# Kernel tuning notes

Hardware: AMD Instinct MI355X
Metric: run time of the kernel (lower is better)

## Reference

```python
import jax, jax.numpy as jnp
import numpy as np

B = 64
NS = [5024, 1257, 315, 80, 21]  # padded vertex counts per mesh level
K = 9                            # spiral length
LAT = 256


def _sconv(x, idx, W, b, elu=True):
    # x: [B, N, F], idx: [N, K] spiral neighbor indices -> gather, GEMM, activation, zero-pad mask
    Bq, N, _ = x.shape
    g = x[:, idx.reshape(-1), :].reshape(Bq, N, -1)  # [B, N, K*F]
    o = g @ W + b
    if elu:
        o = jax.nn.elu(o)
    return o.at[:, -1, :].set(0.0)  # zero the padding vertex


def _pool(M, x):
    # M: [M_out, M_in] dense down/up-sample matrix
    return jnp.einsum('mn,bnf->bmf', M, x)


def _forward(x, s0, s1, s2, s3, D0, D1, D2, D3, U0, U1, U2, U3,
             We0, be0, We1, be1, We2, be2, We3, be3,
             fceW, fceb, fcdW, fcdb,
             Wd0, bd0, Wd1, bd1, Wd2, bd2, Wd3, bd3):
    # encoder: spiral conv + downsample at each level
    h = _pool(D0, _sconv(x, s0, We0, be0))
    h = _pool(D1, _sconv(h, s1, We1, be1))
    h = _pool(D2, _sconv(h, s2, We2, be2))
    h = _pool(D3, _sconv(h, s3, We3, be3))
    z = h.reshape(h.shape[0], -1) @ fceW + fceb          # [B, LAT]
    # decoder: upsample + spiral conv, last conv has identity activation
    h = (z @ fcdW + fcdb).reshape(z.shape[0], NS[4], -1)  # [B, 21, 256]
    h = _sconv(_pool(U3, h), s3, Wd0, bd0)
    h = _sconv(_pool(U2, h), s2, Wd1, bd1)
    h = _sconv(_pool(U1, h), s1, Wd2, bd2)
    h = _sconv(_pool(U0, h), s0, Wd3, bd3, elu=False)
    return h  # [B, 5024, 3]


def setup_inputs() -> dict:
    key = jax.random.key(0)
    ks = iter(jax.random.split(key, 64))
    nrm = lambda shape, s=0.05: jax.random.normal(next(ks), shape, dtype=jnp.float32) * s
    d = {}
    d['x'] = jax.random.normal(next(ks), (B, NS[0], 3), dtype=jnp.float32)
    for i in range(4):
        n = NS[i]
        d[f's{i}'] = jax.random.randint(next(ks), (n, K), 0, n, dtype=jnp.int32).astype(jnp.int64)
    for i in range(4):
        d[f'D{i}'] = nrm((NS[i + 1], NS[i]))
        d[f'U{i}'] = nrm((NS[i], NS[i + 1]))
    enc = [(3, 64), (64, 64), (64, 128), (128, 256)]
    for i, (fi, fo) in enumerate(enc):
        d[f'We{i}'] = nrm((fi * K, fo))
        d[f'be{i}'] = jnp.zeros((fo,), jnp.float32)
    d['fceW'] = nrm((NS[4] * 256, LAT))
    d['fceb'] = jnp.zeros((LAT,), jnp.float32)
    d['fcdW'] = nrm((LAT, NS[4] * 256))
    d['fcdb'] = jnp.zeros((NS[4] * 256,), jnp.float32)
    dec = [(256, 128), (128, 64), (64, 64), (64, 3)]
    for i, (fi, fo) in enumerate(dec):
        d[f'Wd{i}'] = nrm((fi * K, fo))
        d[f'bd{i}'] = jnp.zeros((fo,), jnp.float32)
    return d


def reference(x, s0, s1, s2, s3, D0, D1, D2, D3, U0, U1, U2, U3,
              We0, be0, We1, be1, We2, be2, We3, be3,
              fceW, fceb, fcdW, fcdb,
              Wd0, bd0, Wd1, bd1, Wd2, bd2, Wd3, bd3):
    return _forward(x, s0, s1, s2, s3, D0, D1, D2, D3, U0, U1, U2, U3,
                    We0, be0, We1, be1, We2, be2, We3, be3,
                    fceW, fceb, fcdW, fcdb,
                    Wd0, bd0, Wd1, bd1, Wd2, bd2, Wd3, bd3)
```

## Files before the change

kernel.cpp:

```cpp
#include <hip/hip_runtime.h>
#include <math.h>

typedef __attribute__((ext_vector_type(8))) _Float16 half8;
typedef __attribute__((ext_vector_type(4))) _Float16 half4;
typedef __attribute__((ext_vector_type(4))) float f32x4;
typedef unsigned long long u64;

#define BK 32

#define EPI_NAT  0
#define EPI_TR   1
#define EPI_FCD  2
#define EPI_OUT  3
#define EPI_PART 4

typedef const __attribute__((address_space(1))) void* gas1;
typedef __attribute__((address_space(3))) void* las3;

__device__ __forceinline__ void gl16(const void* g, void* l) {
    __builtin_amdgcn_global_load_lds((gas1)g, (las3)l, 16, 0, 0);
}
template<int N> __device__ __forceinline__ void vwait() {
    asm volatile("s_waitcnt vmcnt(%0)" :: "n"(N) : "memory");
}
__device__ __forceinline__ void barx() {
    asm volatile("" ::: "memory");
    __builtin_amdgcn_s_barrier();
    asm volatile("" ::: "memory");
}

__global__ __launch_bounds__(256, 3) void pool4_k(
    const _Float16* __restrict__ Aw, const _Float16* __restrict__ Bw,
    _Float16* __restrict__ Cp, int M, int Np, u64 c_rs)
{
    constexpr int LPS = 6;

    __shared__ _Float16 sA[2][64][64];
    __shared__ _Float16 sB[2][128][64];

    const int t  = threadIdx.x;
    const int m0 = blockIdx.y * 64;
    const int f0 = blockIdx.x * 128;
    const int lane = t & 63;
    const int wid  = t >> 6;
    const int wm = wid >> 1;
    const int wf = wid & 1;
    const int lm = lane & 15;
    const int lg = lane >> 4;

    f32x4 acc[2][4];
    #pragma unroll
    for (int i = 0; i < 2; ++i)
        #pragma unroll
        for (int j = 0; j < 4; ++j)
            acc[i][j] = (f32x4)0.0f;

    auto stage = [&](int buf, int ks) {
        #pragma unroll
        for (int j = 0; j < 2; ++j) {
            int c   = t + j * 256;
            int row = c >> 3;
            int ch  = (c & 7) ^ (row & 7);
            int rc  = m0 + row; if (rc >= M) rc = M - 1;
            gl16(Aw + (u64)rc * Np + ks * 64 + ch * 8,
                 (_Float16*)&sA[buf][0][0] + (u64)c * 8);
        }
        #pragma unroll
        for (int j = 0; j < 4; ++j) {
            int c   = t + j * 256;
            int row = c >> 3;
            int ch  = (c & 7) ^ (row & 7);
            gl16(Bw + (u64)(f0 + row) * Np + ks * 64 + ch * 8,
                 (_Float16*)&sB[buf][0][0] + (u64)c * 8);
        }
    };

    auto compute = [&](int buf) {
        #pragma unroll
        for (int kh = 0; kh < 2; ++kh) {
            const int ch = (kh * 4 + lg) ^ (lm & 7);
            half8 af[2], bf[4];
            #pragma unroll
            for (int i = 0; i < 2; ++i)
                af[i] = *(const half8*)&sA[buf][wm * 32 + i * 16 + lm][ch * 8];
            #pragma unroll
            for (int j = 0; j < 4; ++j)
                bf[j] = *(const half8*)&sB[buf][wf * 64 + j * 16 + lm][ch * 8];
            #pragma unroll
            for (int i = 0; i < 2; ++i)
                #pragma unroll
                for (int j = 0; j < 4; ++j)
                    acc[i][j] = __builtin_amdgcn_mfma_f32_16x16x32_f16(af[i], bf[j], acc[i][j], 0, 0, 0);
        }
    };

    const int ke = Np / 64;
    stage(0, 0);
    if (1 < ke) stage(1, 1);
    for (int ks = 0; ks < ke; ++ks) {
        if (ke - ks >= 2) vwait<LPS>();
        else              vwait<0>();
        barx();
        compute(ks & 1);
        barx();
        if (ks + 2 < ke) stage(ks & 1, ks + 2);
    }

    #pragma unroll
    for (int j = 0; j < 4; ++j) {
        int fl = f0 + wf * 64 + j * 16 + lm;
        #pragma unroll
        for (int i = 0; i < 2; ++i) {
            #pragma unroll
            for (int r = 0; r < 4; ++r) {
                int m = m0 + wm * 32 + i * 16 + lg * 4 + r;
                if (m < M)
                    Cp[(u64)m * c_rs + fl] = (_Float16)acc[i][j][r];
            }
        }
    }
}

template<int TBM>
__global__ __launch_bounds__(256, 3) void pool2_k(
    const _Float16* __restrict__ Aw, const _Float16* __restrict__ Bw,
    _Float16* __restrict__ Cp, int M, int Np, u64 c_rs)
{
    constexpr int FM  = TBM / 32;
    constexpr int LPS = TBM / 64 + 2;

    __shared__ _Float16 sA[3][TBM][BK];
    __shared__ _Float16 sB[3][128][BK];

    const int t  = threadIdx.x;
    const int m0 = blockIdx.y * TBM;
    const int f0 = blockIdx.x * 128;
    const int lane = t & 63;
    const int wid  = t >> 6;
    const int wm = wid >> 1;
    const int wf = wid & 1;
    const int lm = lane & 15;
    const int lg = lane >> 4;

    f32x4 acc[FM][4];
    #pragma unroll
    for (int i = 0; i < FM; ++i)
        #pragma unroll
        for (int j = 0; j < 4; ++j)
            acc[i][j] = (f32x4)0.0f;

    auto stage = [&](int buf, int ks) {
        #pragma unroll
        for (int j = 0; j < TBM / 64; ++j) {
            int c   = t + j * 256;
            int row = c >> 2;
            int sw  = ((c & 3) ^ ((row >> 1) & 3)) * 8;
            int rc  = m0 + row; if (rc >= M) rc = M - 1;
            gl16(Aw + (u64)rc * Np + ks * BK + sw,
                 (_Float16*)&sA[buf][0][0] + (u64)c * 8);
        }
        #pragma unroll
        for (int j = 0; j < 2; ++j) {
            int c   = t + j * 256;
            int row = c >> 2;
            int sw  = ((c & 3) ^ ((row >> 1) & 3)) * 8;
            gl16(Bw + (u64)(f0 + row) * Np + ks * BK + sw,
                 (_Float16*)&sB[buf][0][0] + (u64)c * 8);
        }
    };

    auto compute = [&](int buf) {
        const int sa = (lg ^ ((lm >> 1) & 3)) * 8;
        half8 af[FM], bf[4];
        #pragma unroll
        for (int i = 0; i < FM; ++i)
            af[i] = *(const half8*)&sA[buf][wm * (FM * 16) + i * 16 + lm][sa];
        #pragma unroll
        for (int j = 0; j < 4; ++j)
            bf[j] = *(const half8*)&sB[buf][wf * 64 + j * 16 + lm][sa];
        #pragma unroll
        for (int i = 0; i < FM; ++i)
            #pragma unroll
            for (int j = 0; j < 4; ++j)
                acc[i][j] = __builtin_amdgcn_mfma_f32_16x16x32_f16(af[i], bf[j], acc[i][j], 0, 0, 0);
    };

    const int ke = Np / BK;
    stage(0, 0);
    if (1 < ke) stage(1, 1);
    if (2 < ke) stage(2, 2);
    int cur = 0;
    for (int ks = 0; ks < ke; ++ks) {
        int rem = ke - ks;
        if (rem >= 3)      vwait<2 * LPS>();
        else if (rem == 2) vwait<LPS>();
        else               vwait<0>();
        barx();
        compute(cur);
        barx();
        if (ks + 3 < ke) stage(cur, ks + 3);
        cur = (cur == 2) ? 0 : cur + 1;
    }

    #pragma unroll
    for (int j = 0; j < 4; ++j) {
        int fl = f0 + wf * 64 + j * 16 + lm;
        #pragma unroll
        for (int i = 0; i < FM; ++i) {
            #pragma unroll
            for (int r = 0; r < 4; ++r) {
                int m = m0 + wm * (FM * 16) + i * 16 + lg * 4 + r;
                if (m < M)
                    Cp[(u64)m * c_rs + fl] = (_Float16)acc[i][j][r];
            }
        }
    }
}

template<int AMODE, int EPI, int TBM, int TBF, int WM, int WF>
__global__ __launch_bounds__(256) void gemm_k(
    const _Float16* __restrict__ Aw, u64 a_rs,
    const int* __restrict__ idx, int FiLog,
    const _Float16* __restrict__ Bw,
    const float* __restrict__ bias,
    void* __restrict__ Cp, u64 c_rs, int Mp_out,
    int M, int Np, int F, int flags, int ksp)
{
    constexpr int FM = TBM / WM / 16;
    constexpr int FF = TBF / WF / 16;
    constexpr int LPS_A = TBM / 64;
    constexpr bool BSM = (TBF < 64);
    constexpr int LPS_B = BSM ? 0 : TBF / 64;
    constexpr int LW0 = LPS_A + (BSM ? 1 : LPS_B);
    constexpr int LWX = LPS_A + LPS_B;
    constexpr int NI = (AMODE == 1 || AMODE == 2) ? TBM : 2;

    __shared__ _Float16 sA[3][TBM][BK];
    __shared__ _Float16 sB[3][TBF][BK];
    __shared__ int sIdx[NI][9];

    const int t  = threadIdx.x;
    const int b  = blockIdx.z;
    const int m0 = blockIdx.y * TBM;
    const int f0 = blockIdx.x * TBF;
    const int lane = t & 63;
    const int wid  = t >> 6;
    const int wm = wid / WF;
    const int wf = wid % WF;
    const int lm = lane & 15;
    const int lg = lane >> 4;
    const int Fi = 1 << FiLog;

    f32x4 acc[FM][FF];
    #pragma unroll
    for (int i = 0; i < FM; ++i)
        #pragma unroll
        for (int j = 0; j < FF; ++j)
            acc[i][j] = (f32x4)0.0f;

    if constexpr (AMODE == 1 || AMODE == 2) {
        for (int i = t; i < TBM * 9; i += 256) {
            int r = i / 9, k = i - r * 9;
            int rc = m0 + r; if (rc >= M) rc = M - 1;
            sIdx[r][k] = idx[rc * 9 + k];
        }
        __syncthreads();
    } else if constexpr (AMODE == 5) {
        if (t < 18) {
            int r = t / 9, k = t - r * 9;
            sIdx[r][k] = idx[((m0 >> 6) + r) * 9 + k];
        }
        __syncthreads();
    }

    auto stage = [&](int buf, int ks) {
        if constexpr (AMODE != 2) {
            #pragma unroll
            for (int j = 0; j < LPS_A; ++j) {
                int c   = t + j * 256;
                int row = c >> 2;
                int sw  = ((c & 3) ^ ((row >> 1) & 3)) * 8;
                int col = ks * BK + sw;
                const _Float16* src;
                if constexpr (AMODE == 3) {
                    int rc = m0 + row; if (rc >= M) rc = M - 1;
                    src = Aw + (u64)rc * Np + col;
                } else if constexpr (AMODE == 1) {
                    int k = col >> FiLog, fi = col & (Fi - 1);
                    src = Aw + (u64)sIdx[row][k] * a_rs + b * Fi + fi;
                } else if constexpr (AMODE == 4) {
                    int k = col >> FiLog, fi = col & (Fi - 1);
                    src = Aw + (u64)k * a_rs + (m0 + row) * Fi + fi;
                } else {
                    int k = col >> FiLog, fi = col & (Fi - 1);
                    int bb = (m0 + row) & 63;
                    src = Aw + (u64)sIdx[row >> 6][k] * a_rs + bb * Fi + fi;
                }
                gl16(src, &sA[buf][row][(c & 3) * 8]);
            }
        }
        if constexpr (!BSM) {
            #pragma unroll
            for (int j = 0; j < LPS_B; ++j) {
                int c   = t + j * 256;
                int row = c >> 2;
                int sw  = ((c & 3) ^ ((row >> 1) & 3)) * 8;
                gl16(Bw + (u64)(f0 + row) * Np + ks * BK + sw, &sB[buf][row][(c & 3) * 8]);
            }
        } else {
            if (wid == 0) {
                int c   = t;
                int row = c >> 2;
                int sw  = ((c & 3) ^ ((row >> 1) & 3)) * 8;
                gl16(Bw + (u64)(f0 + row) * Np + ks * BK + sw, &sB[buf][row][(c & 3) * 8]);
            }
        }
    };

    auto compute = [&](int buf) {
        const int sa = (lg ^ ((lm >> 1) & 3)) * 8;
        half8 af[FM], bf[FF];
        #pragma unroll
        for (int i = 0; i < FM; ++i)
            af[i] = *(const half8*)&sA[buf][wm * (FM * 16) + i * 16 + lm][sa];
        #pragma unroll
        for (int j = 0; j < FF; ++j)
            bf[j] = *(const half8*)&sB[buf][wf * (FF * 16) + j * 16 + lm][sa];
        #pragma unroll
        for (int i = 0; i < FM; ++i)
            #pragma unroll
            for (int j = 0; j < FF; ++j)
                acc[i][j] = __builtin_amdgcn_mfma_f32_16x16x32_f16(af[i], bf[j], acc[i][j], 0, 0, 0);
    };

    if constexpr (AMODE == 2) {
        stage(0, 0);
        stage(1, 1);
        {
            int row = t >> 1;
            int h   = t & 1;
            #pragma unroll
            for (int cc = 0; cc < 4; ++cc) {
                int g0 = h * 8 + cc * 2;
                int g1 = g0 + 1;
                half4 lo = {(_Float16)0,(_Float16)0,(_Float16)0,(_Float16)0};
                half4 hi = lo;
                if (g0 < 9) lo = *(const half4*)(Aw + (u64)sIdx[row][g0] * a_rs + b * 4);
                if (g1 < 9) hi = *(const half4*)(Aw + (u64)sIdx[row][g1] * a_rs + b * 4);
                half8 w;
                #pragma unroll
                for (int q = 0; q < 4; ++q) { w[q] = lo[q]; w[4 + q] = hi[q]; }
                int cp = cc ^ ((row >> 1) & 3);
                *(half8*)&sA[h][row][cp * 8] = w;
            }
        }
        vwait<0>();
        __syncthreads();
        compute(0);
        compute(1);
    } else {
        int kb = 0, ke = Np / BK;
        if constexpr (AMODE == 4) { kb = b * ksp; ke = kb + ksp; }
        stage(0, kb);
        if (kb + 1 < ke) stage(1, kb + 1);
        if (kb + 2 < ke) stage(2, kb + 2);
        int cur = 0;
        for (int ks = kb; ks < ke; ++ks) {
            int rem = ke - ks;
            if (rem >= 3) {
                if constexpr (LW0 == LWX) vwait<2 * LW0>();
                else { if (wid == 0) vwait<2 * LW0>(); else vwait<2 * LWX>(); }
            } else if (rem == 2) {
                if constexpr (LW0 == LWX) vwait<LW0>();
                else { if (wid == 0) vwait<LW0>(); else vwait<LWX>(); }
            } else {
                vwait<0>();
            }
            barx();
            compute(cur);
            barx();
            if (ks + 3 < ke) stage(cur, ks + 3);
            cur = (cur == 2) ? 0 : cur + 1;
        }
    }

    if constexpr (EPI == EPI_TR) {
        #pragma unroll
        for (int j = 0; j < FF; ++j) {
            int fl = f0 + wf * (FF * 16) + j * 16 + lm;
            float bv = (bias != nullptr && fl < F) ? bias[fl] : 0.f;
            #pragma unroll
            for (int i = 0; i < FM; ++i) {
                int mb = m0 + wm * (FM * 16) + i * 16 + lg * 4;
                if (fl < F && mb < Mp_out) {
                    half4 o;
                    #pragma unroll
                    for (int r = 0; r < 4; ++r) {
                        int m = mb + r;
                        float v = acc[i][j][r] + bv;
                        if (flags & 1) v = (v > 0.f) ? v : expm1f(v);
                        o[r] = (m < M && !((flags & 2) && m == M - 1)) ? (_Float16)v : (_Float16)0.f;
                    }
                    *(half4*)&((_Float16*)Cp)[(u64)b * c_rs + (u64)fl * Mp_out + mb] = o;
                }
            }
        }
    } else {
        #pragma unroll
        for (int j = 0; j < FF; ++j) {
            int fl = f0 + wf * (FF * 16) + j * 16 + lm;
            float bv = 0.f;
            if (bias != nullptr && fl < F) bv = bias[fl];
            #pragma unroll
            for (int i = 0; i < FM; ++i) {
                #pragma unroll
                for (int r = 0; r < 4; ++r) {
                    int m = m0 + wm * (FM * 16) + i * 16 + lg * 4 + r;
                    float v = acc[i][j][r] + bv;
                    if (flags & 1) v = (v > 0.f) ? v : expm1f(v);
                    if constexpr (EPI == EPI_NAT) {
                        if (m < M && fl < F)
                            ((_Float16*)Cp)[(u64)m * c_rs + fl] = (_Float16)v;
                    } else if constexpr (EPI == EPI_FCD) {
                        if (m < M && fl < F)
                            ((_Float16*)Cp)[((u64)m * 256 + (fl & 255)) * 32 + (fl >> 8)] = (_Float16)v;
                    } else if constexpr (EPI == EPI_PART) {
                        if (m < M && fl < F)
                            ((float*)Cp)[(u64)b * c_rs + (u64)m * F + fl] = v;
                    } else {
                        if (m < M && fl < F) {
                            int vo = m >> 6, bb = m & 63;
                            float o = ((flags & 2) && vo == Mp_out - 1) ? 0.f : v;
                            ((float*)Cp)[((u64)bb * Mp_out + vo) * 3 + fl] = o;
                        }
                    }
                }
            }
        }
    }
}

struct CvtPtrs { const float* p[18]; };

constexpr int CV_R[18]  = {1257,5024,315,1257,80,315,21,80,  64,64,128,256,256,5376,128,64,64,16};
constexpr int CV_N[18]  = {5024,1257,1257,315,315,80,80,21,  27,576,576,1152,5376,256,2304,1152,576,576};
constexpr int CV_NP[18] = {5120,1280,1280,320,320,96,96,32,  64,576,576,1152,5376,256,2304,1152,576,576};
constexpr int CV_F[18]  = {0,0,0,0,0,0,0,0,  64,64,128,256,256,5376,128,64,64,3};

constexpr u64 cv_elems(int i) { return (u64)CV_R[i] * CV_NP[i]; }
constexpr u64 cv_off(int i) { u64 o = 0; for (int j = 0; j < i; ++j) o += (cv_elems(j) + 255) & ~(u64)255; return o; }
constexpr int cv_blk(int i) { return (int)((cv_elems(i) + 255) >> 8); }
constexpr int cv_start(int i) { int s = 0; for (int j = 0; j < i; ++j) s += cv_blk(j); return s; }

__global__ __launch_bounds__(256) void cvt_all(CvtPtrs ps, _Float16* __restrict__ dst)
{
    const int bx = blockIdx.x, t = threadIdx.x;
    #pragma unroll
    for (int i = 0; i < 18; ++i) {
        if (bx >= cv_start(i) && bx < cv_start(i + 1)) {
            const u64 e = (u64)(bx - cv_start(i)) * 256 + t;
            if (e < cv_elems(i)) {
                const int NP = CV_NP[i], N = CV_N[i], Fo = CV_F[i];
                int row = (int)(e / (u64)NP);
                int col = (int)(e - (u64)row * NP);
                float v = 0.f;
                const float* s = ps.p[i];
                if (i == 8) {
                    int k = col >> 2, c = col & 3;
                    if (c < 3 && k < 9) v = s[(u64)(k * 3 + c) * Fo + row];
                } else if (Fo == 0) {
                    if (col < N) v = s[(u64)row * N + col];
                } else {
                    if (col < N && row < Fo) v = s[(u64)col * Fo + row];
                }
                dst[cv_off(i) + e] = (_Float16)v;
            }
        }
    }
}

__global__ void cvt_x(const float* __restrict__ src, _Float16* __restrict__ dst)
{
    int i = blockIdx.x * 256 + threadIdx.x;
    if (i >= 5024 * 256) return;
    int v = i >> 8;
    int r = i & 255;
    int b = r >> 2, c = r & 3;
    dst[i] = (c < 3) ? (_Float16)src[((u64)b * 5024 + v) * 3 + c] : (_Float16)0.f;
}

__global__ void reduce_fce(const float* __restrict__ part, const float* __restrict__ bias,
                           _Float16* __restrict__ z)
{
    int i = blockIdx.x * 256 + threadIdx.x;
    int fl = i & 255;
    float s = bias[fl];
    #pragma unroll
    for (int p = 0; p < 8; ++p) s += part[(u64)p * 16384 + i];
    z[i] = (_Float16)s;
}

extern "C" void kernel_launch(void* const* d_in, const int* in_sizes, int n_in,
                              void* d_out, int out_size, void* d_ws, size_t ws_size,
                              hipStream_t stream)
{
    const float* x  = (const float*)d_in[0];
    const int* s0 = (const int*)d_in[1];
    const int* s1 = (const int*)d_in[2];
    const int* s2 = (const int*)d_in[3];
    const int* s3 = (const int*)d_in[4];
    const float* be0 = (const float*)d_in[14];
    const float* be1 = (const float*)d_in[16];
    const float* be2 = (const float*)d_in[18];
    const float* be3 = (const float*)d_in[20];
    const float* fceb = (const float*)d_in[22];
    const float* fcdb = (const float*)d_in[24];
    const float* bd0 = (const float*)d_in[26];
    const float* bd1 = (const float*)d_in[28];
    const float* bd2 = (const float*)d_in[30];
    const float* bd3 = (const float*)d_in[32];

    _Float16* W = (_Float16*)d_ws;
    size_t off = 0;
    auto alloc = [&](size_t e) { size_t o = off; off += (e + 255) & ~(size_t)255; return o; };

    const size_t oActV = alloc((size_t)5024 * 4096);
    const size_t oActT = alloc((size_t)4096 * 5120);
    const size_t oZ    = alloc((size_t)64 * 256);
    const size_t oPart = alloc((size_t)8 * 64 * 256 * 2);
    const size_t oU3in = alloc((size_t)16384 * 32);
    const size_t oXp   = alloc((size_t)5024 * 256);
    const size_t oCvt  = alloc((size_t)(cv_off(17) + ((cv_elems(17) + 255) & ~(u64)255)));
    auto wofs = [&](int i) { return oCvt + (size_t)cv_off(i); };

    cvt_x<<<dim3(5024), 256, 0, stream>>>(x, W + oXp);
    {
        CvtPtrs ps;
        ps.p[0] = (const float*)d_in[5];
        ps.p[1] = (const float*)d_in[6];
        ps.p[2] = (const float*)d_in[7];
        ps.p[3] = (const float*)d_in[8];
        ps.p[4] = (const float*)d_in[9];
        ps.p[5] = (const float*)d_in[10];
        ps.p[6] = (const float*)d_in[11];
        ps.p[7] = (const float*)d_in[12];
        ps.p[8] = (const float*)d_in[13];
        ps.p[9] = (const float*)d_in[15];
        ps.p[10] = (const float*)d_in[17];
        ps.p[11] = (const float*)d_in[19];
        ps.p[12] = (const float*)d_in[21];
        ps.p[13] = (const float*)d_in[23];
        ps.p[14] = (const float*)d_in[25];
        ps.p[15] = (const float*)d_in[27];
        ps.p[16] = (const float*)d_in[29];
        ps.p[17] = (const float*)d_in[31];
        cvt_all<<<dim3(cv_start(18)), 256, 0, stream>>>(ps, W + oCvt);
    }
    hipMemsetAsync(W + oU3in, 0, (size_t)16384 * 32 * sizeof(_Float16), stream);

    #define GEMM(AM, EP, BM_, BF_, WM_, WF_, gx, gy, gz, Aw_, ars_, idx_, FiL_, Bw_, bias_, Cp_, crs_, Mp_, M_, Np_, F_, fl_, ksp_) \
        gemm_k<AM, EP, BM_, BF_, WM_, WF_><<<dim3(gx, gy, gz), 256, 0, stream>>>( \
            Aw_, ars_, idx_, FiL_, Bw_, bias_, Cp_, crs_, Mp_, M_, Np_, F_, fl_, ksp_)
    #define POOL(TBM_, gx, gy, Aw_, Bw_, Cp_, M_, Np_, crs_) \
        pool2_k<TBM_><<<dim3(gx, gy), 256, 0, stream>>>(Aw_, Bw_, Cp_, M_, Np_, crs_)
    #define POOL4(gx, gy, Aw_, Bw_, Cp_, M_, Np_, crs_) \
        pool4_k<<<dim3(gx, gy), 256, 0, stream>>>(Aw_, Bw_, Cp_, M_, Np_, crs_)

    GEMM(2, EPI_TR, 128, 64, 2, 2, 1, 40, 64, W + oXp, 256, s0, 0,
         W + wofs(8), be0, W + oActT, (u64)64 * 5120, 5120, 5024, 64, 64, 3, 0);
    POOL4(32, 20, W + wofs(0), W + oActT, W + oActV, 1257, 5120, 4096);
    GEMM(1, EPI_TR, 128, 64, 2, 2, 1, 10, 64, W + oActV, 4096, s1, 6,
         W + wofs(9), be1, W + oActT, (u64)64 * 1280, 1280, 1257, 576, 64, 3, 0);
    POOL(64, 32, 5, W + wofs(2), W + oActT, W + oActV, 315, 1280, 4096);
    GEMM(1, EPI_TR, 128, 64, 2, 2, 2, 3, 64, W + oActV, 4096, s2, 6,
         W + wofs(10), be2, W + oActT, (u64)128 * 320, 320, 315, 576, 128, 3, 0);
    POOL(64, 64, 2, W + wofs(4), W + oActT, W + oActV, 80, 320, 8192);
    GEMM(1, EPI_TR, 128, 64, 2, 2, 4, 1, 64, W + oActV, 8192, s3, 7,
         W + wofs(11), be3, W + oActT, (u64)256 * 96, 96, 80, 1152, 256, 3, 0);
    POOL(64, 128, 1, W + wofs(6), W + oActT, W + oActV, 21, 96, 16384);
    GEMM(4, EPI_PART, 64, 64, 2, 2, 4, 1, 8, W + oActV, 16384, nullptr, 8,
         W + wofs(12), nullptr, W + oPart, (u64)64 * 256, 0, 64, 5376, 256, 0, 21);
    reduce_fce<<<dim3(64), 256, 0, stream>>>((const float*)(W + oPart), fceb, W + oZ);
    GEMM(3, EPI_FCD, 64, 128, 2, 2, 42, 1, 1, W + oZ, 0, nullptr, 0,
         W + wofs(13), fcdb, W + oU3in, 0, 0, 64, 256, 5376, 0, 0);
    POOL(64, 128, 2, W + wofs(7), W + oU3in, W + oActV, 80, 32, 16384);
    GEMM(1, EPI_TR, 128, 64, 2, 2, 2, 1, 64, W + oActV, 16384, s3, 8,
         W + wofs(14), bd0, W + oActT, (u64)128 * 96, 96, 80, 2304, 128, 3, 0);
    POOL(64, 64, 5, W + wofs(5), W + oActT, W + oActV, 315, 96, 8192);
    GEMM(1, EPI_TR, 128, 64, 2, 2, 1, 3, 64, W + oActV, 8192, s2, 7,
         W + wofs(15), bd1, W + oActT, (u64)64 * 320, 320, 315, 1152, 64, 3, 0);
    POOL4(32, 20, W + wofs(3), W + oActT, W + oActV, 1257, 320, 4096);
    GEMM(1, EPI_TR, 128, 64, 2, 2, 1, 10, 64, W + oActV, 4096, s1, 6,
         W + wofs(16), bd2, W + oActT, (u64)64 * 1280, 1280, 1257, 576, 64, 3, 0);
    POOL4(32, 79, W + wofs(1), W + oActT, W + oActV, 5024, 1280, 4096);
    GEMM(5, EPI_OUT, 128, 16, 4, 1, 1, 2512, 1, W + oActV, 4096, s0, 6,
         W + wofs(17), bd3, d_out, 0, 5024, 321536, 576, 3, 2, 0);
    #undef GEMM
    #undef POOL
    #undef POOL4
}
```

Measured before the change: 505.8 us.

## Add dedicated spiral-conv GEMM kernel with BK=64 double buffering and wider MFMA

Adds a specialised sconv4_k kernel for the gathered spiral-convolution GEMMs. It uses a 64-wide K tile with double buffering, an XOR-swizzled LDS layout and the 16x16x32 f16 MFMA, and writes vectorised half4 outputs with a fused bias/ELU/pad-zero epilogue. It replaces the generic gemm_k AMODE 1 path for six conv layers and moves two pooling launches to the pool4 kernel. The aim is fewer K iterations and barriers plus cheaper stores. In exchange it requires Np to be a multiple of 64 and holds more LDS per block.

```diff
diff --git a/kernel.cpp b/kernel.cpp
--- a/kernel.cpp
+++ b/kernel.cpp
@@ -116,6 +116,123 @@
                 int m = m0 + wm * 32 + i * 16 + lg * 4 + r;
                 if (m < M)
                     Cp[(u64)m * c_rs + fl] = (_Float16)acc[i][j][r];
+            }
+        }
+    }
+}
+
+template<int TBM, int TBF, int WM, int WF>
+__global__ __launch_bounds__(256) void sconv4_k(
+    const _Float16* __restrict__ Aw, u64 a_rs,
+    const int* __restrict__ idx, int FiLog,
+    const _Float16* __restrict__ Bw,
+    const float* __restrict__ bias,
+    _Float16* __restrict__ Cp, u64 c_rs, int Mp_out,
+    int M, int Np, int F, int flags)
+{
+    constexpr int FM = TBM / WM / 16;
+    constexpr int FF = TBF / WF / 16;
+    constexpr int LPS = TBM / 32 + TBF / 32;
+
+    __shared__ _Float16 sA[2][TBM][64];
+    __shared__ _Float16 sB[2][TBF][64];
+    __shared__ int sIdx[TBM][9];
+
+    const int t  = threadIdx.x;
+    const int b  = blockIdx.z;
+    const int m0 = blockIdx.y * TBM;
+    const int f0 = blockIdx.x * TBF;
+    const int lane = t & 63;
+    const int wid  = t >> 6;
+    const int wm = wid / WF;
+    const int wf = wid % WF;
+    const int lm = lane & 15;
+    const int lg = lane >> 4;
+    const int Fi = 1 << FiLog;
+
+    f32x4 acc[FM][FF];
+    #pragma unroll
+    for (int i = 0; i < FM; ++i)
+        #pragma unroll
+        for (int j = 0; j < FF; ++j)
+            acc[i][j] = (f32x4)0.0f;
+
+    for (int i = t; i < TBM * 9; i += 256) {
+        int r = i / 9, k = i - r * 9;
+        int rc = m0 + r; if (rc >= M) rc = M - 1;
+        sIdx[r][k] = idx[rc * 9 + k];
+    }
+    __syncthreads();
+
+    auto stage = [&](int buf, int ks) {
+        #pragma unroll
+        for (int j = 0; j < TBM / 32; ++j) {
+            int c   = t + j * 256;
+            int row = c >> 3;
+            int ch  = (c & 7) ^ (row & 7);
+            int col = ks * 64 + ch * 8;
+            int k = col >> FiLog, fi = col & (Fi - 1);
+            gl16(Aw + (u64)sIdx[row][k] * a_rs + b * Fi + fi,
+                 (_Float16*)&sA[buf][0][0] + (u64)c * 8);
+        }
+        #pragma unroll
+        for (int j = 0; j < TBF / 32; ++j) {
+            int c   = t + j * 256;
+            int row = c >> 3;
+            int ch  = (c & 7) ^ (row & 7);
+            gl16(Bw + (u64)(f0 + row) * Np + ks * 64 + ch * 8,
+                 (_Float16*)&sB[buf][0][0] + (u64)c * 8);
+        }
+    };
+
+    auto compute = [&](int buf) {
+        #pragma unroll
+        for (int kh = 0; kh < 2; ++kh) {
+            const int ch = (kh * 4 + lg) ^ (lm & 7);
+            half8 af[FM], bf[FF];
+            #pragma unroll
+            for (int i = 0; i < FM; ++i)
+                af[i] = *(const half8*)&sA[buf][wm * (FM * 16) + i * 16 + lm][ch * 8];
+            #pragma unroll
+            for (int j = 0; j < FF; ++j)
+                bf[j] = *(const half8*)&sB[buf][wf * (FF * 16) + j * 16 + lm][ch * 8];
+            #pragma unroll
+            for (int i = 0; i < FM; ++i)
+                #pragma unroll
+                for (int j = 0; j < FF; ++j)
+                    acc[i][j] = __builtin_amdgcn_mfma_f32_16x16x32_f16(af[i], bf[j], acc[i][j], 0, 0, 0);
+        }
+    };
+
+    const int ke = Np / 64;
+    stage(0, 0);
+    if (1 < ke) stage(1, 1);
+    for (int ks = 0; ks < ke; ++ks) {
+        if (ke - ks >= 2) vwait<LPS>();
+        else              vwait<0>();
+        barx();
+        compute(ks & 1);
+        barx();
+        if (ks + 2 < ke) stage(ks & 1, ks + 2);
+    }
+
+    #pragma unroll
+    for (int j = 0; j < FF; ++j) {
+        int fl = f0 + wf * (FF * 16) + j * 16 + lm;
+        float bv = (bias != nullptr && fl < F) ? bias[fl] : 0.f;
+        #pragma unroll
+        for (int i = 0; i < FM; ++i) {
+            int mb = m0 + wm * (FM * 16) + i * 16 + lg * 4;
+            if (fl < F && mb < Mp_out) {
+                half4 o;
+                #pragma unroll
+                for (int r = 0; r < 4; ++r) {
+                    int m = mb + r;
+                    float v = acc[i][j][r] + bv;
+                    if (flags & 1) v = (v > 0.f) ? v : expm1f(v);
+                    o[r] = (m < M && !((flags & 2) && m == M - 1)) ? (_Float16)v : (_Float16)0.f;
+                }
+                *(half4*)&Cp[(u64)b * c_rs + (u64)fl * Mp_out + mb] = o;
             }
         }
     }
@@ -233,7 +350,7 @@
     constexpr int LPS_B = BSM ? 0 : TBF / 64;
     constexpr int LW0 = LPS_A + (BSM ? 1 : LPS_B);
     constexpr int LWX = LPS_A + LPS_B;
-    constexpr int NI = (AMODE == 1 || AMODE == 2) ? TBM : 2;
+    constexpr int NI = (AMODE == 2) ? TBM : 2;
 
     __shared__ _Float16 sA[3][TBM][BK];
     __shared__ _Float16 sB[3][TBF][BK];
@@ -258,7 +375,7 @@
         for (int j = 0; j < FF; ++j)
             acc[i][j] = (f32x4)0.0f;
 
-    if constexpr (AMODE == 1 || AMODE == 2) {
+    if constexpr (AMODE == 2) {
         for (int i = t; i < TBM * 9; i += 256) {
             int r = i / 9, k = i - r * 9;
             int rc = m0 + r; if (rc >= M) rc = M - 1;
@@ -285,9 +402,6 @@
                 if constexpr (AMODE == 3) {
                     int rc = m0 + row; if (rc >= M) rc = M - 1;
                     src = Aw + (u64)rc * Np + col;
-                } else if constexpr (AMODE == 1) {
-                    int k = col >> FiLog, fi = col & (Fi - 1);
-                    src = Aw + (u64)sIdx[row][k] * a_rs + b * Fi + fi;
                 } else if constexpr (AMODE == 4) {
                     int k = col >> FiLog, fi = col & (Fi - 1);
                     src = Aw + (u64)k * a_rs + (m0 + row) * Fi + fi;
@@ -561,6 +675,9 @@
     #define GEMM(AM, EP, BM_, BF_, WM_, WF_, gx, gy, gz, Aw_, ars_, idx_, FiL_, Bw_, bias_, Cp_, crs_, Mp_, M_, Np_, F_, fl_, ksp_) \
         gemm_k<AM, EP, BM_, BF_, WM_, WF_><<<dim3(gx, gy, gz), 256, 0, stream>>>( \
             Aw_, ars_, idx_, FiL_, Bw_, bias_, Cp_, crs_, Mp_, M_, Np_, F_, fl_, ksp_)
+    #define SC4(BM_, BF_, WM_, WF_, gx, gy, Aw_, ars_, idx_, FiL_, Bw_, bias_, Cp_, crs_, Mp_, M_, Np_, F_, fl_) \
+        sconv4_k<BM_, BF_, WM_, WF_><<<dim3(gx, gy, 64), 256, 0, stream>>>( \
+            Aw_, ars_, idx_, FiL_, Bw_, bias_, Cp_, crs_, Mp_, M_, Np_, F_, fl_)
     #define POOL(TBM_, gx, gy, Aw_, Bw_, Cp_, M_, Np_, crs_) \
         pool2_k<TBM_><<<dim3(gx, gy), 256, 0, stream>>>(Aw_, Bw_, Cp_, M_, Np_, crs_)
     #define POOL4(gx, gy, Aw_, Bw_, Cp_, M_, Np_, crs_) \
@@ -569,14 +686,14 @@
     GEMM(2, EPI_TR, 128, 64, 2, 2, 1, 40, 64, W + oXp, 256, s0, 0,
          W + wofs(8), be0, W + oActT, (u64)64 * 5120, 5120, 5024, 64, 64, 3, 0);
     POOL4(32, 20, W + wofs(0), W + oActT, W + oActV, 1257, 5120, 4096);
-    GEMM(1, EPI_TR, 128, 64, 2, 2, 1, 10, 64, W + oActV, 4096, s1, 6,
-         W + wofs(9), be1, W + oActT, (u64)64 * 1280, 1280, 1257, 576, 64, 3, 0);
-    POOL(64, 32, 5, W + wofs(2), W + oActT, W + oActV, 315, 1280, 4096);
-    GEMM(1, EPI_TR, 128, 64, 2, 2, 2, 3, 64, W + oActV, 4096, s2, 6,
-         W + wofs(10), be2, W + oActT, (u64)128 * 320, 320, 315, 576, 128, 3, 0);
-    POOL(64, 64, 2, W + wofs(4), W + oActT, W + oActV, 80, 320, 8192);
-    GEMM(1, EPI_TR, 128, 64, 2, 2, 4, 1, 64, W + oActV, 8192, s3, 7,
-         W + wofs(11), be3, W + oActT, (u64)256 * 96, 96, 80, 1152, 256, 3, 0);
+    SC4(128, 64, 2, 2, 1, 10, W + oActV, 4096, s1, 6,
+        W + wofs(9), be1, W + oActT, (u64)64 * 1280, 1280, 1257, 576, 64, 3);
+    POOL4(32, 5, W + wofs(2), W + oActT, W + oActV, 315, 1280, 4096);
+    SC4(128, 64, 2, 2, 2, 3, W + oActV, 4096, s2, 6,
+        W + wofs(10), be2, W + oActT, (u64)128 * 320, 320, 315, 576, 128, 3);
+    POOL4(64, 2, W + wofs(4), W + oActT, W + oActV, 80, 320, 8192);
+    SC4(128, 64, 2, 2, 4, 1, W + oActV, 8192, s3, 7,
+        W + wofs(11), be3, W + oActT, (u64)256 * 96, 96, 80, 1152, 256, 3);
     POOL(64, 128, 1, W + wofs(6), W + oActT, W + oActV, 21, 96, 16384);
     GEMM(4, EPI_PART, 64, 64, 2, 2, 4, 1, 8, W + oActV, 16384, nullptr, 8,
          W + wofs(12), nullptr, W + oPart, (u64)64 * 256, 0, 64, 5376, 256, 0, 21);
@@ -584,18 +701,19 @@
     GEMM(3, EPI_FCD, 64, 128, 2, 2, 42, 1, 1, W + oZ, 0, nullptr, 0,
          W + wofs(13), fcdb, W + oU3in, 0, 0, 64, 256, 5376, 0, 0);
     POOL(64, 128, 2, W + wofs(7), W + oU3in, W + oActV, 80, 32, 16384);
-    GEMM(1, EPI_TR, 128, 64, 2, 2, 2, 1, 64, W + oActV, 16384, s3, 8,
-         W + wofs(14), bd0, W + oActT, (u64)128 * 96, 96, 80, 2304, 128, 3, 0);
+    SC4(128, 64, 2, 2, 2, 1, W + oActV, 16384, s3, 8,
+        W + wofs(14), bd0, W + oActT, (u64)128 * 96, 96, 80, 2304, 128, 3);
     POOL(64, 64, 5, W + wofs(5), W + oActT, W + oActV, 315, 96, 8192);
-    GEMM(1, EPI_TR, 128, 64, 2, 2, 1, 3, 64, W + oActV, 8192, s2, 7,
-         W + wofs(15), bd1, W + oActT, (u64)64 * 320, 320, 315, 1152, 64, 3, 0);
+    SC4(128, 64, 2, 2, 1, 3, W + oActV, 8192, s2, 7,
+        W + wofs(15), bd1, W + oActT, (u64)64 * 320, 320, 315, 1152, 64, 3);
     POOL4(32, 20, W + wofs(3), W + oActT, W + oActV, 1257, 320, 4096);
-    GEMM(1, EPI_TR, 128, 64, 2, 2, 1, 10, 64, W + oActV, 4096, s1, 6,
-         W + wofs(16), bd2, W + oActT, (u64)64 * 1280, 1280, 1257, 576, 64, 3, 0);
+    SC4(128, 64, 2, 2, 1, 10, W + oActV, 4096, s1, 6,
+        W + wofs(16), bd2, W + oActT, (u64)64 * 1280, 1280, 1257, 576, 64, 3);
     POOL4(32, 79, W + wofs(1), W + oActT, W + oActV, 5024, 1280, 4096);
     GEMM(5, EPI_OUT, 128, 16, 4, 1, 1, 2512, 1, W + oActV, 4096, s0, 6,
          W + wofs(17), bd3, d_out, 0, 5024, 321536, 576, 3, 2, 0);
     #undef GEMM
+    #undef SC4
     #undef POOL
     #undef POOL4
 }
```

Result: faster. 487.3 us (-3.7%).
